# Optimization experiments

Hardware: AMD Instinct MI355X
Metric: run time of the kernel (lower is better)

The kernel has to match this reference:

```python
import jax, jax.numpy as jnp
import numpy as np


def setup_inputs() -> dict:
    key = jax.random.key(0)
    k1, k2, k3 = jax.random.split(key, 3)
    B, H, W = 32, 512, 512
    N = H * W  # tokens
    K = 32768  # positive_trials
    decision_scores = jax.random.normal(k1, (B, N, 2), dtype=jnp.float32)
    s_map = jax.random.uniform(k2, (B, 1, H, W), dtype=jnp.float32)
    # uniform noise for gumbel sampling, kept away from {0,1} for log stability
    u = jax.random.uniform(k3, (B, N, 2), dtype=jnp.float32, minval=1e-6, maxval=1.0 - 1e-6)
    return {"decision_scores": decision_scores, "s_map": s_map, "u": u, "positive_trials": K}


def reference(decision_scores, s_map, u, positive_trials):
    B, N, _ = decision_scores.shape
    # gumbel_softmax(hard=False, tau=1): softmax(logits + gumbel_noise)
    gumbel = -jnp.log(-jnp.log(u))
    logp = jax.nn.log_softmax(decision_scores + gumbel, axis=-1)  # [B, N, 2]
    # soft_decisions = p[..., 0]
    # Tokenizer: [B, 1, H, W] -> [B, N, 1]; use channel 0 as salience score.
    scores = s_map.reshape(B, 1, -1).transpose(0, 2, 1)[..., 0]  # [B, N]
    # argsort descending, take top-k indices == lax.top_k indices
    _, idx = jax.lax.top_k(scores, positive_trials)  # [B, K]
    trials = jnp.zeros((B, N), dtype=decision_scores.dtype)
    trials = trials.at[jnp.arange(B)[:, None], idx].set(1.0)  # scatter ones
    # BCE(sum): -sum(t*log(p) + (1-t)*log(1-p)); with 2-class softmax, 1-p0 = p1.
    # torch BCE clamps log terms at -100.
    logp0 = jnp.clip(logp[..., 0], -100.0)
    logp1 = jnp.clip(logp[..., 1], -100.0)
    loss = -jnp.sum(trials * logp0 + (1.0 - trials) * logp1)
    return loss
```

## Files before the change

### kernel.cpp

```cpp
#include <hip/hip_runtime.h>

#define NB    4096
#define CAPL  1024
#define BATCH 32
#define NTOK  262144
#define HPB   8
#define ABLK  (BATCH * HPB)
#define ATHR  1024

typedef float f4 __attribute__((ext_vector_type(4)));

__device__ __forceinline__ int bucket_of(float v) {
    int b = (int)(v * (float)NB);
    return b > NB - 1 ? NB - 1 : b;
}

__device__ __forceinline__ void token_terms(float d0, float d1, float u0, float u1,
                                            float& dd, float& bce) {
    float g0 = -__logf(-__logf(u0));
    float g1 = -__logf(-__logf(u1));
    dd = (d0 + g0) - (d1 + g1);
    float l = __logf(1.f + __expf(-fabsf(dd)));
    bce = fminf(l + fmaxf(dd, 0.f), 100.f);
}

__global__ __launch_bounds__(1024) void fused_kernel(
        const float* __restrict__ ds, const float* __restrict__ u,
        const float* __restrict__ smap,
        unsigned short* __restrict__ hist_part, float* __restrict__ dsum_part,
        float* __restrict__ bce_part) {
    __shared__ int   lh[NB];
    __shared__ float ldd[NB];
    for (int i = threadIdx.x; i < NB; i += ATHR) { lh[i] = 0; ldd[i] = 0.f; }
    __syncthreads();
    const int b  = blockIdx.x >> 3;
    const int cb = blockIdx.x & 7;
    const size_t Q0 = (size_t)b * (NTOK / 4) + (size_t)cb * (NTOK / 4 / HPB);
    const f4* s4 = (const f4*)smap + Q0;
    const f4* d4 = (const f4*)ds + 2 * Q0;
    const f4* u4 = (const f4*)u  + 2 * Q0;
    float bce = 0.f;
    for (int k = 0; k < 8; k++) {
        int q = threadIdx.x + k * ATHR;
        f4 sv = s4[q];
        f4 dA = __builtin_nontemporal_load(&d4[2 * q]);
        f4 dB = __builtin_nontemporal_load(&d4[2 * q + 1]);
        f4 uA = __builtin_nontemporal_load(&u4[2 * q]);
        f4 uB = __builtin_nontemporal_load(&u4[2 * q + 1]);
        float dd0, dd1, dd2, dd3, t0, t1, t2, t3;
        token_terms(dA.x, dA.y, uA.x, uA.y, dd0, t0);
        token_terms(dA.z, dA.w, uA.z, uA.w, dd1, t1);
        token_terms(dB.x, dB.y, uB.x, uB.y, dd2, t2);
        token_terms(dB.z, dB.w, uB.z, uB.w, dd3, t3);
        bce += (t0 + t1) + (t2 + t3);
        atomicAdd(&lh[bucket_of(sv.x)], 1); atomicAdd(&ldd[bucket_of(sv.x)], dd0);
        atomicAdd(&lh[bucket_of(sv.y)], 1); atomicAdd(&ldd[bucket_of(sv.y)], dd1);
        atomicAdd(&lh[bucket_of(sv.z)], 1); atomicAdd(&ldd[bucket_of(sv.z)], dd2);
        atomicAdd(&lh[bucket_of(sv.w)], 1); atomicAdd(&ldd[bucket_of(sv.w)], dd3);
    }
    __syncthreads();
    unsigned short* hp = hist_part + (size_t)blockIdx.x * NB;
    float*          dp = dsum_part + (size_t)blockIdx.x * NB;
    for (int i = threadIdx.x; i < NB; i += ATHR) {
        hp[i] = (unsigned short)lh[i];
        dp[i] = ldd[i];
    }
    for (int off = 32; off > 0; off >>= 1) bce += __shfl_down(bce, off, 64);
    __shared__ float red[16];
    const int lane = threadIdx.x & 63, wv = threadIdx.x >> 6;
    if (lane == 0) red[wv] = bce;
    __syncthreads();
    if (threadIdx.x == 0) {
        float s = 0.f;
        for (int w = 0; w < 16; w++) s += red[w];
        bce_part[blockIdx.x] = s;
    }
}

__global__ __launch_bounds__(1024) void selcorr_kernel(
        const float* __restrict__ smap, const float* __restrict__ ds,
        const float* __restrict__ u,
        const unsigned short* __restrict__ hist_part, const float* __restrict__ dsum_part,
        const int* __restrict__ kptr, float* __restrict__ corr) {
    __shared__ int   lh[NB];
    __shared__ float ldd[NB];
    __shared__ int   suf[1024 + 1];
    __shared__ float cv[CAPL];
    __shared__ int   ci[CAPL];
    __shared__ float cdd[CAPL];
    __shared__ float csel[CAPL];
    __shared__ int   s_cnt, s_tb, s_R;
    __shared__ float fred1[16], fred2[16];
    const int b = blockIdx.x, t = threadIdx.x;
    if (t == 0) s_cnt = 0;

    const unsigned short* hp = hist_part + (size_t)b * HPB * NB;
    const float*          dp = dsum_part + (size_t)b * HPB * NB;
    for (int i = t; i < NB; i += 1024) {
        int s = 0; float f = 0.f;
        #pragma unroll
        for (int p = 0; p < HPB; p++) { s += hp[(size_t)p * NB + i]; f += dp[(size_t)p * NB + i]; }
        lh[i] = s; ldd[i] = f;
    }
    __syncthreads();

    const int base = t * 4;
    int c = lh[base] + lh[base + 1] + lh[base + 2] + lh[base + 3];
    suf[t] = c;
    if (t == 0) suf[1024] = 0;
    __syncthreads();
    for (int off = 1; off < 1024; off <<= 1) {
        int v = suf[t] + ((t + off < 1024) ? suf[t + off] : 0);
        __syncthreads();
        suf[t] = v;
        __syncthreads();
    }
    const int K = *kptr;
    {
        int cum = suf[t + 1];
        #pragma unroll
        for (int i = 3; i >= 0; i--) {
            int hb = lh[base + i];
            if (cum < K && cum + hb >= K) { s_tb = base + i; s_R = K - cum; }
            cum += hb;
        }
    }
    __syncthreads();
    const int tb = s_tb, R = s_R;

    float s1p = 0.f;
    for (int i = t; i < NB; i += 1024) if (i > tb) s1p += ldd[i];
    for (int off = 32; off > 0; off >>= 1) s1p += __shfl_down(s1p, off, 64);
    const int lane = t & 63, wv = t >> 6;
    if (lane == 0) fred1[wv] = s1p;

    const f4* s4 = (const f4*)smap + (size_t)b * (NTOK / 4);
    for (int k = 0; k < 64; k++) {
        int q = t + k * 1024;
        f4 v = s4[q];
        float vals[4] = {v.x, v.y, v.z, v.w};
        #pragma unroll
        for (int j = 0; j < 4; j++) {
            if (bucket_of(vals[j]) == tb) {
                int p = atomicAdd(&s_cnt, 1);
                if (p < CAPL) { cv[p] = vals[j]; ci[p] = 4 * q + j; }
            }
        }
    }
    __syncthreads();
    int M = s_cnt;
    const bool ovf = (M > CAPL);
    if (ovf) M = CAPL;

    for (int i = t; i < M; i += 1024) {
        const int n = ci[i];
        float2 dpair = ((const float2*)ds)[(size_t)b * NTOK + n];
        float2 upair = ((const float2*)u)[(size_t)b * NTOK + n];
        float g0 = -__logf(-__logf(upair.x));
        float g1 = -__logf(-__logf(upair.y));
        cdd[i] = (dpair.x + g0) - (dpair.y + g1);
    }
    for (int i = t; i < CAPL; i += 1024) csel[i] = 0.f;
    __syncthreads();
    if (!ovf) {
        for (int i = t; i < M; i += 1024) {
            float vi = cv[i]; int ii = ci[i];
            int r = 0;
            for (int j = 0; j < M; j++) {
                float vj = cv[j];
                r += (vj > vi) || (vj == vi && ci[j] < ii);
            }
            if (r < R) csel[i] = cdd[i];
        }
    }
    __syncthreads();
    float s2p = csel[t];
    for (int off = 32; off > 0; off >>= 1) s2p += __shfl_down(s2p, off, 64);
    if (lane == 0) fred2[wv] = s2p;
    __syncthreads();
    if (t == 0) {
        float S1 = 0.f, S2 = 0.f;
        for (int w = 0; w < 16; w++) { S1 += fred1[w]; S2 += fred2[w]; }
        if (ovf) S2 = ldd[tb];
        corr[b] = S1 + S2;
    }
}

__global__ __launch_bounds__(256) void final_kernel(const float* __restrict__ bce_part,
                                                    const float* __restrict__ corr,
                                                    float* __restrict__ out) {
    const int t = threadIdx.x;
    float a = bce_part[t];
    for (int off = 32; off > 0; off >>= 1) a += __shfl_down(a, off, 64);
    __shared__ float red[4];
    const int lane = t & 63, wv = t >> 6;
    if (lane == 0) red[wv] = a;
    __syncthreads();
    if (t == 0) {
        float s = red[0] + red[1] + red[2] + red[3];
        float cc = 0.f;
        for (int i = 0; i < BATCH; i++) cc += corr[i];
        out[0] = s - cc;
    }
}

extern "C" void kernel_launch(void* const* d_in, const int* in_sizes, int n_in,
                              void* d_out, int out_size, void* d_ws, size_t ws_size,
                              hipStream_t stream) {
    const float* ds   = (const float*)d_in[0];
    const float* smap = (const float*)d_in[1];
    const float* u    = (const float*)d_in[2];
    const int*   kptr = (const int*)d_in[3];

    float*          dsum_part = (float*)d_ws;
    unsigned short* hist_part = (unsigned short*)(dsum_part + (size_t)ABLK * NB);
    float*          bce_part  = (float*)(hist_part + (size_t)ABLK * NB);
    float*          corr      = bce_part + ABLK;

    fused_kernel<<<ABLK, ATHR, 0, stream>>>(ds, u, smap, hist_part, dsum_part, bce_part);
    selcorr_kernel<<<BATCH, 1024, 0, stream>>>(smap, ds, u, hist_part, dsum_part, kptr, corr);
    final_kernel<<<1, 256, 0, stream>>>(bce_part, corr, (float*)d_out);
}
```

Baseline: 218.8 us.

## Split selection into select, collect, refine kernels to parallelize threshold-bucket scan

The single per-batch selection kernel, which rescanned all of s_map with only 32 blocks, is split into three kernels. A select kernel finds the threshold bucket and the partial sum above it. A 1024-block collect kernel gathers threshold-bucket candidates into global buffers using global atomics. A refine kernel ranks the candidates and gathers the ds/u values only for the selected tokens. The aim is to spread the 32 MB s_map rescan across the whole GPU. The cost is two extra launches, global-atomic contention, and a larger candidate capacity for the quadratic ranking.

```diff
diff --git a/kernel.cpp b/kernel.cpp
--- a/kernel.cpp
+++ b/kernel.cpp
@@ -1,7 +1,7 @@
 #include <hip/hip_runtime.h>
 
 #define NB    4096
-#define CAPL  1024
+#define CAP   4096
 #define BATCH 32
 #define NTOK  262144
 #define HPB   8
@@ -77,23 +77,17 @@
     }
 }
 
-__global__ __launch_bounds__(1024) void selcorr_kernel(
-        const float* __restrict__ smap, const float* __restrict__ ds,
-        const float* __restrict__ u,
+__global__ __launch_bounds__(1024) void select_kernel(
         const unsigned short* __restrict__ hist_part, const float* __restrict__ dsum_part,
-        const int* __restrict__ kptr, float* __restrict__ corr) {
+        const int* __restrict__ kptr, int* __restrict__ tbR, int* __restrict__ cnt,
+        float* __restrict__ S1) {
     __shared__ int   lh[NB];
     __shared__ float ldd[NB];
-    __shared__ int   suf[1024 + 1];
-    __shared__ float cv[CAPL];
-    __shared__ int   ci[CAPL];
-    __shared__ float cdd[CAPL];
-    __shared__ float csel[CAPL];
-    __shared__ int   s_cnt, s_tb, s_R;
-    __shared__ float fred1[16], fred2[16];
+    __shared__ int   suf[1025];
+    __shared__ int   s_tb;
+    __shared__ float fred[16];
     const int b = blockIdx.x, t = threadIdx.x;
-    if (t == 0) s_cnt = 0;
-
+    if (t == 0) cnt[b] = 0;
     const unsigned short* hp = hist_part + (size_t)b * HPB * NB;
     const float*          dp = dsum_part + (size_t)b * HPB * NB;
     for (int i = t; i < NB; i += 1024) {
@@ -103,7 +97,6 @@
         lh[i] = s; ldd[i] = f;
     }
     __syncthreads();
-
     const int base = t * 4;
     int c = lh[base] + lh[base + 1] + lh[base + 2] + lh[base + 3];
     suf[t] = c;
@@ -121,69 +114,108 @@
         #pragma unroll
         for (int i = 3; i >= 0; i--) {
             int hb = lh[base + i];
-            if (cum < K && cum + hb >= K) { s_tb = base + i; s_R = K - cum; }
+            if (cum < K && cum + hb >= K) {
+                s_tb = base + i;
+                tbR[2 * b] = base + i; tbR[2 * b + 1] = K - cum;
+            }
             cum += hb;
         }
     }
     __syncthreads();
-    const int tb = s_tb, R = s_R;
-
+    const int tb = s_tb;
     float s1p = 0.f;
     for (int i = t; i < NB; i += 1024) if (i > tb) s1p += ldd[i];
     for (int off = 32; off > 0; off >>= 1) s1p += __shfl_down(s1p, off, 64);
     const int lane = t & 63, wv = t >> 6;
-    if (lane == 0) fred1[wv] = s1p;
-
-    const f4* s4 = (const f4*)smap + (size_t)b * (NTOK / 4);
-    for (int k = 0; k < 64; k++) {
-        int q = t + k * 1024;
-        f4 v = s4[q];
-        float vals[4] = {v.x, v.y, v.z, v.w};
+    if (lane == 0) fred[wv] = s1p;
+    __syncthreads();
+    if (t == 0) {
+        float s = 0.f;
+        for (int w = 0; w < 16; w++) s += fred[w];
+        S1[b] = s;
+    }
+}
+
+__global__ __launch_bounds__(256) void collect_kernel(const float* __restrict__ smap,
+        const int* __restrict__ tbR, int* __restrict__ cnt,
+        float* __restrict__ cval, int* __restrict__ cidx) {
+    const int b = blockIdx.x >> 5, cb = blockIdx.x & 31;
+    const int tb = tbR[2 * b];
+    const int t = cb * 256 + threadIdx.x;
+    const f4* src = (const f4*)(smap + (size_t)b * NTOK) + (size_t)t * 8;
+    const int n0 = t * 32;
+    #pragma unroll
+    for (int j = 0; j < 8; j++) {
+        f4 v = src[j];
+        float vv[4] = {v.x, v.y, v.z, v.w};
         #pragma unroll
-        for (int j = 0; j < 4; j++) {
-            if (bucket_of(vals[j]) == tb) {
-                int p = atomicAdd(&s_cnt, 1);
-                if (p < CAPL) { cv[p] = vals[j]; ci[p] = 4 * q + j; }
+        for (int s = 0; s < 4; s++) {
+            if (bucket_of(vv[s]) == tb) {
+                int p = atomicAdd(&cnt[b], 1);
+                if (p < CAP) {
+                    cval[b * CAP + p] = vv[s];
+                    cidx[b * CAP + p] = n0 + 4 * j + s;
+                }
             }
         }
     }
-    __syncthreads();
-    int M = s_cnt;
-    const bool ovf = (M > CAPL);
-    if (ovf) M = CAPL;
-
-    for (int i = t; i < M; i += 1024) {
-        const int n = ci[i];
-        float2 dpair = ((const float2*)ds)[(size_t)b * NTOK + n];
-        float2 upair = ((const float2*)u)[(size_t)b * NTOK + n];
-        float g0 = -__logf(-__logf(upair.x));
-        float g1 = -__logf(-__logf(upair.y));
-        cdd[i] = (dpair.x + g0) - (dpair.y + g1);
-    }
-    for (int i = t; i < CAPL; i += 1024) csel[i] = 0.f;
-    __syncthreads();
-    if (!ovf) {
-        for (int i = t; i < M; i += 1024) {
-            float vi = cv[i]; int ii = ci[i];
-            int r = 0;
-            for (int j = 0; j < M; j++) {
-                float vj = cv[j];
-                r += (vj > vi) || (vj == vi && ci[j] < ii);
-            }
-            if (r < R) csel[i] = cdd[i];
-        }
-    }
-    __syncthreads();
-    float s2p = csel[t];
+}
+
+__global__ __launch_bounds__(256) void refine_kernel(
+        const float* __restrict__ ds, const float* __restrict__ u,
+        const float* __restrict__ dsum_part, const int* __restrict__ tbR,
+        const int* __restrict__ cnt, const float* __restrict__ cval,
+        const int* __restrict__ cidx, const float* __restrict__ S1,
+        float* __restrict__ corr) {
+    const int b = blockIdx.x, t = threadIdx.x;
+    const int R = tbR[2 * b + 1];
+    int M = cnt[b];
+    const bool ovf = (M > CAP);
+    if (M > CAP) M = CAP;
+    __shared__ float sv[CAP];
+    __shared__ int   si[CAP];
+    __shared__ float csel[CAP];
+    for (int i = t; i < CAP; i += 256) csel[i] = 0.f;
+    for (int i = t; i < M; i += 256) {
+        sv[i] = cval[b * CAP + i];
+        si[i] = cidx[b * CAP + i];
+    }
+    __syncthreads();
+    if (ovf || R > M || R < 1) {
+        if (t == 0) {
+            const int tb = tbR[2 * b];
+            float s2 = 0.f;
+            for (int p = 0; p < HPB; p++)
+                s2 += dsum_part[(size_t)(b * HPB + p) * NB + tb];
+            corr[b] = S1[b] + s2;
+        }
+        return;
+    }
+    for (int i = t; i < M; i += 256) {
+        float vi = sv[i]; int ii = si[i];
+        int r = 0;
+        for (int j = 0; j < M; j++) {
+            float vj = sv[j];
+            r += (vj > vi) || (vj == vi && si[j] < ii);
+        }
+        if (r < R) {
+            float2 dpair = ((const float2*)ds)[(size_t)b * NTOK + ii];
+            float2 upair = ((const float2*)u)[(size_t)b * NTOK + ii];
+            float g0 = -__logf(-__logf(upair.x));
+            float g1 = -__logf(-__logf(upair.y));
+            csel[i] = (dpair.x + g0) - (dpair.y + g1);
+        }
+    }
+    __syncthreads();
+    float s2p = 0.f;
+    #pragma unroll
+    for (int k = 0; k < CAP / 256; k++) s2p += csel[t + k * 256];
     for (int off = 32; off > 0; off >>= 1) s2p += __shfl_down(s2p, off, 64);
-    if (lane == 0) fred2[wv] = s2p;
-    __syncthreads();
-    if (t == 0) {
-        float S1 = 0.f, S2 = 0.f;
-        for (int w = 0; w < 16; w++) { S1 += fred1[w]; S2 += fred2[w]; }
-        if (ovf) S2 = ldd[tb];
-        corr[b] = S1 + S2;
-    }
+    __shared__ float fred[4];
+    const int lane = t & 63, wv = t >> 6;
+    if (lane == 0) fred[wv] = s2p;
+    __syncthreads();
+    if (t == 0) corr[b] = S1[b] + (fred[0] + fred[1] + fred[2] + fred[3]);
 }
 
 __global__ __launch_bounds__(256) void final_kernel(const float* __restrict__ bce_part,
@@ -214,10 +246,17 @@
 
     float*          dsum_part = (float*)d_ws;
     unsigned short* hist_part = (unsigned short*)(dsum_part + (size_t)ABLK * NB);
-    float*          bce_part  = (float*)(hist_part + (size_t)ABLK * NB);
-    float*          corr      = bce_part + ABLK;
+    float* bce_part = (float*)(hist_part + (size_t)ABLK * NB);
+    int*   tbR      = (int*)(bce_part + ABLK);
+    int*   cnt      = tbR + 2 * BATCH;
+    float* S1       = (float*)(cnt + BATCH);
+    float* corr     = S1 + BATCH;
+    float* cval     = corr + BATCH;
+    int*   cidx     = (int*)(cval + (size_t)BATCH * CAP);
 
     fused_kernel<<<ABLK, ATHR, 0, stream>>>(ds, u, smap, hist_part, dsum_part, bce_part);
-    selcorr_kernel<<<BATCH, 1024, 0, stream>>>(smap, ds, u, hist_part, dsum_part, kptr, corr);
+    select_kernel<<<BATCH, 1024, 0, stream>>>(hist_part, dsum_part, kptr, tbR, cnt, S1);
+    collect_kernel<<<1024, 256, 0, stream>>>(smap, tbR, cnt, cval, cidx);
+    refine_kernel<<<BATCH, 256, 0, stream>>>(ds, u, dsum_part, tbR, cnt, cval, cidx, S1, corr);
     final_kernel<<<1, 256, 0, stream>>>(bce_part, corr, (float*)d_out);
 }
```

Result: faster. 211.3 us (-3.4%).
